# Kernel optimization log

Hardware: AMD Instinct MI355X
Metric: run time of the kernel (lower is better)

The kernel has to match this reference:

```python
import jax, jax.numpy as jnp
import numpy as np

B, D, H, K = 32768, 784, 500, 50


def setup_inputs() -> dict:
    key = jax.random.key(0)
    ks = jax.random.split(key, 12)
    s = 0.02  # weight init scale
    return {
        "x": jax.random.uniform(ks[0], (B, D), dtype=jnp.float32),
        "u": jax.random.uniform(ks[1], (B, K), dtype=jnp.float32),
        "enc_w1": jax.random.normal(ks[2], (D, H), dtype=jnp.float32) * s,
        "enc_b1": jnp.zeros((H,), jnp.float32),
        "w_alpha": jax.random.normal(ks[3], (H, K), dtype=jnp.float32) * s,
        "b_alpha": jnp.zeros((K,), jnp.float32),
        "w_beta": jax.random.normal(ks[4], (H, K), dtype=jnp.float32) * s,
        "b_beta": jnp.zeros((K,), jnp.float32),
        "dec_w1": jax.random.normal(ks[5], (K, H), dtype=jnp.float32) * s,
        "dec_b1": jnp.zeros((H,), jnp.float32),
        "dec_w2": jax.random.normal(ks[6], (H, D), dtype=jnp.float32) * s,
        "dec_b2": jnp.zeros((D,), jnp.float32),
    }


def reference(x, u, enc_w1, enc_b1, w_alpha, b_alpha, w_beta, b_beta,
              dec_w1, dec_b1, dec_w2, dec_b2):
    # encode
    h = jax.nn.relu(x @ enc_w1 + enc_b1)                       # [B,H]
    alpha = jax.nn.softplus(h @ w_alpha + b_alpha)             # [B,K] > 0
    beta = jax.nn.softplus(h @ w_beta + b_beta)                # [B,K] > 0
    # Kumaraswamy inverse-CDF sample: v = (1 - u^(1/beta))^(1/alpha)
    v = (1.0 - u ** (1.0 / beta)) ** (1.0 / alpha)             # [B,K]
    # stick-breaking: pi[k] = v[k] * prod_{j<k}(1 - v[j])  (exclusive cumprod)
    cp = jnp.cumprod(1.0 - v, axis=-1)                         # [B,K]
    pi = v * jnp.concatenate([jnp.ones_like(v[:, :1]), cp[:, :-1]], axis=-1)
    # decode
    hd = jax.nn.relu(pi @ dec_w1 + dec_b1)                     # [B,H]
    recon_x = jax.nn.sigmoid(hd @ dec_w2 + dec_b2)             # [B,D]
    return recon_x, alpha, beta
```

## Files before the change

kernel.cpp:

```cpp
#include <hip/hip_runtime.h>
#include <math.h>


typedef __bf16 bf16x8 __attribute__((ext_vector_type(8)));
typedef float f32x4 __attribute__((ext_vector_type(4)));

#define BATCH 32768
#define BM 128
#define BN 128
#define BK 64
#define NTHR 512

__device__ __forceinline__ unsigned short bf16_bits(float f) {
    __bf16 b = (__bf16)f;
    return __builtin_bit_cast(unsigned short, b);
}

__device__ __forceinline__ void gll16(const void* src, void* ldsdst) {
    __builtin_amdgcn_global_load_lds(
        (const __attribute__((address_space(1))) unsigned int*)src,
        (__attribute__((address_space(3))) unsigned int*)ldsdst,
        16, 0, 0);
}

template<int MODE>
__global__ __launch_bounds__(NTHR, 4) void mfma_gemm(
    const unsigned short* __restrict__ A,
    const unsigned short* __restrict__ Bt,
    const float* __restrict__ bias,
    void* __restrict__ Cv,
    int Kpad, int lda, int ldc, int Nreal, int nbx)
{
    __shared__ unsigned short As[BM * BK];
    __shared__ unsigned short Bs[BN * BK];

    const int nwg = gridDim.x;
    const int orig = blockIdx.x;
    const int q = nwg >> 3, r8 = nwg & 7;
    const int xcd = orig & 7;
    const int chunkbase = (xcd < r8) ? xcd * (q + 1) : r8 * (q + 1) + (xcd - r8) * q;
    const int wgid = chunkbase + (orig >> 3);
    const int bn = wgid % nbx;
    const size_t block_m = (size_t)(wgid / nbx) * BM;
    const int block_n = bn * BN;

    const int tid = threadIdx.x;
    const int l = tid & 63;
    const int wid = tid >> 6;
    const int wr = wid >> 2, wc = wid & 3;

    const int lr = l & 15;
    const int kh = l >> 4;

    f32x4 acc[4][2] = {};

    for (int k0 = 0; k0 < Kpad; k0 += BK) {
        #pragma unroll
        for (int i = 0; i < 2; ++i) {
            int chunk = wid * 2 + i;
            int gid = chunk * 64 + l;
            int r = gid >> 3;
            int kgs = (gid & 7) ^ (r & 7);
            gll16(Bt + (size_t)(block_n + r) * Kpad + k0 + kgs * 8, Bs + chunk * 512);
        }
        #pragma unroll
        for (int i = 0; i < 2; ++i) {
            int chunk = wid * 2 + i;
            int gid = chunk * 64 + l;
            int r = gid >> 3;
            int kgs = (gid & 7) ^ (r & 7);
            gll16(A + (block_m + r) * (size_t)lda + k0 + kgs * 8, As + chunk * 512);
        }
        __syncthreads();

        #pragma unroll
        for (int s = 0; s < 2; ++s) {
            bf16x8 af[4], bf[2];
            #pragma unroll
            for (int mi = 0; mi < 4; ++mi) {
                int row = wr * 64 + mi * 16 + lr;
                int g = (s * 4 + kh) ^ (row & 7);
                af[mi] = *(const bf16x8*)(As + row * 64 + g * 8);
            }
            #pragma unroll
            for (int ni = 0; ni < 2; ++ni) {
                int row = wc * 32 + ni * 16 + lr;
                int g = (s * 4 + kh) ^ (row & 7);
                bf[ni] = *(const bf16x8*)(Bs + row * 64 + g * 8);
            }
            #pragma unroll
            for (int mi = 0; mi < 4; ++mi)
                #pragma unroll
                for (int ni = 0; ni < 2; ++ni)
                    acc[mi][ni] = __builtin_amdgcn_mfma_f32_16x16x32_bf16(
                        af[mi], bf[ni], acc[mi][ni], 0, 0, 0);
        }
        __syncthreads();
    }

    const int rg = (l >> 4) * 4;
    #pragma unroll
    for (int mi = 0; mi < 4; ++mi) {
        #pragma unroll
        for (int ni = 0; ni < 2; ++ni) {
            int gn = block_n + wc * 32 + ni * 16 + lr;
            float bs = bias[gn];
            #pragma unroll
            for (int j = 0; j < 4; ++j) {
                long gm = block_m + wr * 64 + mi * 16 + rg + j;
                float z = acc[mi][ni][j] + bs;
                if (MODE == 0) {
                    z = fmaxf(z, 0.f);
                    ((unsigned short*)Cv)[gm * ldc + gn] = bf16_bits(z);
                } else if (MODE == 1) {
                    z = (z > 0.f) ? z + __logf(1.f + __expf(-z))
                                  : __logf(1.f + __expf(z));
                    float* out = (float*)Cv;
                    if (gn < 50)       out[gm * 50 + gn] = z;
                    else if (gn < 100) out[(size_t)BATCH * 50 + gm * 50 + (gn - 50)] = z;
                } else {
                    if (gn < Nreal) {
                        z = __fdividef(1.f, 1.f + __expf(-z));
                        ((float*)Cv)[gm * Nreal + gn] = z;
                    }
                }
            }
        }
    }
}

__global__ __launch_bounds__(NTHR, 4) void sample_gemm4(
    const float* __restrict__ u, const float* __restrict__ alpha,
    const float* __restrict__ beta,
    const unsigned short* __restrict__ dw1b,
    const float* __restrict__ biasd1,
    unsigned short* __restrict__ hdb)
{
    __shared__ unsigned short Pi[128 * 64];
    __shared__ unsigned short Wd[2][128 * 64];

    const int tid = threadIdx.x;
    const int l = tid & 63;
    const int wid = tid >> 6;

    const int nwg = gridDim.x;
    const int orig = blockIdx.x;
    const int q = nwg >> 3, r8 = nwg & 7;
    const int xcd = orig & 7;
    const int chunkbase = (xcd < r8) ? xcd * (q + 1) : r8 * (q + 1) + (xcd - r8) * q;
    const int wgid = chunkbase + (orig >> 3);
    const size_t block_m = (size_t)wgid * 128;

    auto stageW = [&](int j, int buf) {
        #pragma unroll
        for (int i = 0; i < 2; ++i) {
            int chunk = wid * 2 + i;
            int gid = chunk * 64 + l;
            int r = gid >> 3;
            int kgs = (gid & 7) ^ (r & 7);
            gll16(dw1b + (size_t)(j * 128 + r) * 64 + kgs * 8,
                  &Wd[buf][chunk * 512]);
        }
    };

    stageW(0, 0);

    for (int rr = 0; rr < 16; ++rr) {
        int row = wid * 16 + rr;
        size_t grow = block_m + row;
        float v = 0.f, w = 1.f;
        if (l < 50) {
            float a = alpha[grow * 50 + l];
            float b = beta[grow * 50 + l];
            float uu = u[grow * 50 + l];
            float t = exp2f(__fdividef(log2f(uu), b));
            v = exp2f(__fdividef(log2f(1.f - t), a));
            w = 1.f - v;
        }
        float p = w;
        #pragma unroll
        for (int off = 1; off < 64; off <<= 1) {
            float t2 = __shfl_up(p, off, 64);
            if (l >= off) p *= t2;
        }
        float ex = __shfl_up(p, 1, 64);
        if (l == 0) ex = 1.f;
        float pi = (l < 50) ? v * ex : 0.f;
        Pi[row * 64 + (((l >> 3) ^ (row & 7)) << 3) + (l & 7)] = bf16_bits(pi);
    }
    __syncthreads();

    const int lr = l & 15, kh = l >> 4;
    const int wr = wid >> 2, wc = wid & 3;
    const int rg = (l >> 4) * 4;

    for (int j = 0; j < 4; ++j) {
        if (j < 3) stageW(j + 1, (j + 1) & 1);
        f32x4 acc[4][2] = {};
        const unsigned short* W = Wd[j & 1];
        #pragma unroll
        for (int s = 0; s < 2; ++s) {
            bf16x8 af[4], bf[2];
            #pragma unroll
            for (int mi = 0; mi < 4; ++mi) {
                int row = wr * 64 + mi * 16 + lr;
                int g = (s * 4 + kh) ^ (row & 7);
                af[mi] = *(const bf16x8*)(Pi + row * 64 + g * 8);
            }
            #pragma unroll
            for (int ni = 0; ni < 2; ++ni) {
                int row = wc * 32 + ni * 16 + lr;
                int g = (s * 4 + kh) ^ (row & 7);
                bf[ni] = *(const bf16x8*)(W + row * 64 + g * 8);
            }
            #pragma unroll
            for (int mi = 0; mi < 4; ++mi)
                #pragma unroll
                for (int ni = 0; ni < 2; ++ni)
                    acc[mi][ni] = __builtin_amdgcn_mfma_f32_16x16x32_bf16(
                        af[mi], bf[ni], acc[mi][ni], 0, 0, 0);
        }
        #pragma unroll
        for (int mi = 0; mi < 4; ++mi) {
            #pragma unroll
            for (int ni = 0; ni < 2; ++ni) {
                int gn = j * 128 + wc * 32 + ni * 16 + lr;
                float bs = biasd1[gn];
                #pragma unroll
                for (int jj = 0; jj < 4; ++jj) {
                    long gm = block_m + wr * 64 + mi * 16 + rg + jj;
                    float z = fmaxf(acc[mi][ni][jj] + bs, 0.f);
                    hdb[gm * 512 + gn] = bf16_bits(z);
                }
            }
        }
        __syncthreads();
    }
}

__global__ __launch_bounds__(256) void cast_x(
    const float* __restrict__ x, unsigned short* __restrict__ xb)
{
    int gid = blockIdx.x * 256 + threadIdx.x;
    int r = gid / 104;
    int c = gid - r * 104;
    union { __bf16 b[8]; uint4 u; } pk;
    if (c < 98) {
        const float4* p = (const float4*)(x + (size_t)r * 784 + c * 8);
        float4 f0 = p[0], f1 = p[1];
        pk.b[0] = (__bf16)f0.x; pk.b[1] = (__bf16)f0.y;
        pk.b[2] = (__bf16)f0.z; pk.b[3] = (__bf16)f0.w;
        pk.b[4] = (__bf16)f1.x; pk.b[5] = (__bf16)f1.y;
        pk.b[6] = (__bf16)f1.z; pk.b[7] = (__bf16)f1.w;
    } else {
        pk.u = make_uint4(0, 0, 0, 0);
    }
    *(uint4*)(xb + (size_t)r * 832 + c * 8) = pk.u;
}

__global__ __launch_bounds__(256) void prep_all(
    const float* __restrict__ enc_w1, const float* __restrict__ enc_b1,
    const float* __restrict__ Wa, const float* __restrict__ ba,
    const float* __restrict__ Wb, const float* __restrict__ bb,
    const float* __restrict__ dec_w1, const float* __restrict__ dec_b1,
    const float* __restrict__ dec_w2, const float* __restrict__ dec_b2,
    unsigned short* __restrict__ w1b, float* __restrict__ bias1,
    unsigned short* __restrict__ wab, float* __restrict__ biasab,
    unsigned short* __restrict__ dw1b, float* __restrict__ biasd1,
    unsigned short* __restrict__ dw2b, float* __restrict__ biasd2)
{
    int bid = blockIdx.x;
    int t = threadIdx.x;
    if (bid < 1664) {
        int idx = bid * 256 + t;
        int n = idx / 832, k = idx - n * 832;
        float v = (n < 500 && k < 784) ? enc_w1[(size_t)k * 500 + n] : 0.f;
        w1b[idx] = bf16_bits(v);
        if (k == 0) bias1[n] = (n < 500) ? enc_b1[n] : 0.f;
    } else if (bid < 1920) {
        int idx = (bid - 1664) * 256 + t;
        int n = idx >> 9, k = idx & 511;
        float v = 0.f;
        if (k < 500) {
            if (n < 50)       v = Wa[(size_t)k * 50 + n];
            else if (n < 100) v = Wb[(size_t)k * 50 + (n - 50)];
        }
        wab[idx] = bf16_bits(v);
        if (k == 0) biasab[n] = (n < 50) ? ba[n] : ((n < 100) ? bb[n - 50] : 0.f);
    } else if (bid < 2048) {
        int idx = (bid - 1920) * 256 + t;
        int n = idx >> 6, k = idx & 63;
        float v = (n < 500 && k < 50) ? dec_w1[(size_t)k * 500 + n] : 0.f;
        dw1b[idx] = bf16_bits(v);
        if (k == 0) biasd1[n] = (n < 500) ? dec_b1[n] : 0.f;
    } else {
        int idx = (bid - 2048) * 256 + t;
        int n = idx >> 9, k = idx & 511;
        float v = (n < 784 && k < 500) ? dec_w2[(size_t)k * 784 + n] : 0.f;
        dw2b[idx] = bf16_bits(v);
        if (k == 0) biasd2[n] = (n < 784) ? dec_b2[n] : 0.f;
    }
}

extern "C" void kernel_launch(void* const* d_in, const int* in_sizes, int n_in,
                              void* d_out, int out_size, void* d_ws, size_t ws_size,
                              hipStream_t stream) {
    const float* x       = (const float*)d_in[0];
    const float* u       = (const float*)d_in[1];
    const float* enc_w1  = (const float*)d_in[2];
    const float* enc_b1  = (const float*)d_in[3];
    const float* w_alpha = (const float*)d_in[4];
    const float* b_alpha = (const float*)d_in[5];
    const float* w_beta  = (const float*)d_in[6];
    const float* b_beta  = (const float*)d_in[7];
    const float* dec_w1  = (const float*)d_in[8];
    const float* dec_b1  = (const float*)d_in[9];
    const float* dec_w2  = (const float*)d_in[10];
    const float* dec_b2  = (const float*)d_in[11];

    const int D = 784;

    float* out   = (float*)d_out;
    float* recon = out;
    float* alpha = out + (size_t)BATCH * D;

    unsigned short* xb = (unsigned short*)d_out;

    char* ws = (char*)d_ws;
    unsigned short* w1b  = (unsigned short*)(ws);
    unsigned short* wab  = (unsigned short*)(ws + 851968);
    unsigned short* dw1b = (unsigned short*)(ws + 983040);
    unsigned short* dw2b = (unsigned short*)(ws + 1048576);
    float* bias1  = (float*)(ws + 1966080);
    float* biasab = (float*)(ws + 1968128);
    float* biasd1 = (float*)(ws + 1970688);
    float* biasd2 = (float*)(ws + 1972736);
    unsigned short* h    = (unsigned short*)(ws + 2097152);
    unsigned short* hdb  = h;

    cast_x<<<dim3(BATCH * 104 / 256), 256, 0, stream>>>(x, xb);
    prep_all<<<dim3(3840), 256, 0, stream>>>(
        enc_w1, enc_b1, w_alpha, b_alpha, w_beta, b_beta,
        dec_w1, dec_b1, dec_w2, dec_b2,
        w1b, bias1, wab, biasab, dw1b, biasd1, dw2b, biasd2);

    mfma_gemm<0><<<dim3((512 / BN) * (BATCH / BM)), NTHR, 0, stream>>>(
        xb, w1b, bias1, h, 832, 832, 512, 500, 512 / BN);

    mfma_gemm<1><<<dim3(BATCH / BM), NTHR, 0, stream>>>(
        h, wab, biasab, alpha, 512, 512, 0, 100, 1);

    sample_gemm4<<<dim3(BATCH / 128), NTHR, 0, stream>>>(
        u, alpha, alpha + (size_t)BATCH * 50, dw1b, biasd1, hdb);

    mfma_gemm<2><<<dim3((896 / BN) * (BATCH / BM)), NTHR, 0, stream>>>(
        hdb, dw2b, biasd2, recon, 512, 512, 784, 784, 896 / BN);
}
```

Baseline: 150.8 us.

## Fuse alpha/beta GEMM with sampling and decoder GEMM; merge cast into prep

The softplus alpha/beta GEMM, the Kumaraswamy sampling with stick-breaking, and the first decoder GEMM now run in one kernel. Alpha and beta stay in LDS for the sampling step instead of being read back from global memory, though they are still written out as results. The x-cast kernel is folded into the weight-prep launch as extra blocks, so two kernel launches disappear in total. The fused kernel needs about 112KB of LDS, which reduces how many workgroups fit on each CU. The GEMM phase is also serialized with the sampling phase inside each block.

```diff
diff --git a/kernel.cpp b/kernel.cpp
--- a/kernel.cpp
+++ b/kernel.cpp
@@ -21,6 +21,13 @@
         (const __attribute__((address_space(1))) unsigned int*)src,
         (__attribute__((address_space(3))) unsigned int*)ldsdst,
         16, 0, 0);
+}
+
+__device__ __forceinline__ int xcd_swz(int orig, int nwg) {
+    int q = nwg >> 3, r8 = nwg & 7;
+    int xcd = orig & 7;
+    int chunkbase = (xcd < r8) ? xcd * (q + 1) : r8 * (q + 1) + (xcd - r8) * q;
+    return chunkbase + (orig >> 3);
 }
 
 template<int MODE>
@@ -34,12 +41,7 @@
     __shared__ unsigned short As[BM * BK];
     __shared__ unsigned short Bs[BN * BK];
 
-    const int nwg = gridDim.x;
-    const int orig = blockIdx.x;
-    const int q = nwg >> 3, r8 = nwg & 7;
-    const int xcd = orig & 7;
-    const int chunkbase = (xcd < r8) ? xcd * (q + 1) : r8 * (q + 1) + (xcd - r8) * q;
-    const int wgid = chunkbase + (orig >> 3);
+    const int wgid = xcd_swz(blockIdx.x, gridDim.x);
     const int bn = wgid % nbx;
     const size_t block_m = (size_t)(wgid / nbx) * BM;
     const int block_n = bn * BN;
@@ -48,7 +50,6 @@
     const int l = tid & 63;
     const int wid = tid >> 6;
     const int wr = wid >> 2, wc = wid & 3;
-
     const int lr = l & 15;
     const int kh = l >> 4;
 
@@ -72,7 +73,6 @@
             gll16(A + (block_m + r) * (size_t)lda + k0 + kgs * 8, As + chunk * 512);
         }
         __syncthreads();
-
         #pragma unroll
         for (int s = 0; s < 2; ++s) {
             bf16x8 af[4], bf[2];
@@ -112,12 +112,6 @@
                 if (MODE == 0) {
                     z = fmaxf(z, 0.f);
                     ((unsigned short*)Cv)[gm * ldc + gn] = bf16_bits(z);
-                } else if (MODE == 1) {
-                    z = (z > 0.f) ? z + __logf(1.f + __expf(-z))
-                                  : __logf(1.f + __expf(z));
-                    float* out = (float*)Cv;
-                    if (gn < 50)       out[gm * 50 + gn] = z;
-                    else if (gn < 100) out[(size_t)BATCH * 50 + gm * 50 + (gn - 50)] = z;
                 } else {
                     if (gn < Nreal) {
                         z = __fdividef(1.f, 1.f + __expf(-z));
@@ -129,51 +123,129 @@
     }
 }
 
-__global__ __launch_bounds__(NTHR, 4) void sample_gemm4(
-    const float* __restrict__ u, const float* __restrict__ alpha,
-    const float* __restrict__ beta,
+__global__ __launch_bounds__(NTHR, 2) void mid_fused(
+    const unsigned short* __restrict__ h,
+    const unsigned short* __restrict__ wab,
+    const float* __restrict__ biasab,
+    const float* __restrict__ u,
     const unsigned short* __restrict__ dw1b,
     const float* __restrict__ biasd1,
+    float* __restrict__ outAB,
     unsigned short* __restrict__ hdb)
 {
-    __shared__ unsigned short Pi[128 * 64];
-    __shared__ unsigned short Wd[2][128 * 64];
+    __shared__ __align__(16) unsigned char smem[114688];
+    float* ab = (float*)smem;
+    unsigned short* Pi = (unsigned short*)(smem + 65536);
+    unsigned short* Wd = (unsigned short*)(smem + 81920);
+    unsigned short* As = (unsigned short*)(smem + 81920);
+    unsigned short* Bs = (unsigned short*)(smem + 81920 + 16384);
 
     const int tid = threadIdx.x;
     const int l = tid & 63;
     const int wid = tid >> 6;
-
-    const int nwg = gridDim.x;
-    const int orig = blockIdx.x;
-    const int q = nwg >> 3, r8 = nwg & 7;
-    const int xcd = orig & 7;
-    const int chunkbase = (xcd < r8) ? xcd * (q + 1) : r8 * (q + 1) + (xcd - r8) * q;
-    const int wgid = chunkbase + (orig >> 3);
+    const int wr = wid >> 2, wc = wid & 3;
+    const int lr = l & 15;
+    const int kh = l >> 4;
+    const int rg = (l >> 4) * 4;
+
+    const int wgid = xcd_swz(blockIdx.x, gridDim.x);
     const size_t block_m = (size_t)wgid * 128;
 
-    auto stageW = [&](int j, int buf) {
+    {
+        f32x4 acc[4][2] = {};
+        for (int k0 = 0; k0 < 512; k0 += BK) {
+            #pragma unroll
+            for (int i = 0; i < 2; ++i) {
+                int chunk = wid * 2 + i;
+                int gid = chunk * 64 + l;
+                int r = gid >> 3;
+                int kgs = (gid & 7) ^ (r & 7);
+                gll16(wab + (size_t)r * 512 + k0 + kgs * 8, Bs + chunk * 512);
+            }
+            #pragma unroll
+            for (int i = 0; i < 2; ++i) {
+                int chunk = wid * 2 + i;
+                int gid = chunk * 64 + l;
+                int r = gid >> 3;
+                int kgs = (gid & 7) ^ (r & 7);
+                gll16(h + (block_m + r) * 512 + k0 + kgs * 8, As + chunk * 512);
+            }
+            __syncthreads();
+            #pragma unroll
+            for (int s = 0; s < 2; ++s) {
+                bf16x8 af[4], bf[2];
+                #pragma unroll
+                for (int mi = 0; mi < 4; ++mi) {
+                    int row = wr * 64 + mi * 16 + lr;
+                    int g = (s * 4 + kh) ^ (row & 7);
+                    af[mi] = *(const bf16x8*)(As + row * 64 + g * 8);
+                }
+                #pragma unroll
+                for (int ni = 0; ni < 2; ++ni) {
+                    int row = wc * 32 + ni * 16 + lr;
+                    int g = (s * 4 + kh) ^ (row & 7);
+                    bf[ni] = *(const bf16x8*)(Bs + row * 64 + g * 8);
+                }
+                #pragma unroll
+                for (int mi = 0; mi < 4; ++mi)
+                    #pragma unroll
+                    for (int ni = 0; ni < 2; ++ni)
+                        acc[mi][ni] = __builtin_amdgcn_mfma_f32_16x16x32_bf16(
+                            af[mi], bf[ni], acc[mi][ni], 0, 0, 0);
+            }
+            __syncthreads();
+        }
+
         #pragma unroll
         for (int i = 0; i < 2; ++i) {
             int chunk = wid * 2 + i;
             int gid = chunk * 64 + l;
             int r = gid >> 3;
             int kgs = (gid & 7) ^ (r & 7);
-            gll16(dw1b + (size_t)(j * 128 + r) * 64 + kgs * 8,
-                  &Wd[buf][chunk * 512]);
-        }
-    };
-
-    stageW(0, 0);
-
+            gll16(dw1b + (size_t)r * 64 + kgs * 8, Wd + chunk * 512);
+        }
+
+        #pragma unroll
+        for (int mi = 0; mi < 4; ++mi) {
+            #pragma unroll
+            for (int ni = 0; ni < 2; ++ni) {
+                int gn = wc * 32 + ni * 16 + lr;
+                float bs = biasab[gn];
+                #pragma unroll
+                for (int j = 0; j < 4; ++j) {
+                    int lm = wr * 64 + mi * 16 + rg + j;
+                    long gm = block_m + lm;
+                    float z = acc[mi][ni][j] + bs;
+                    z = (z > 0.f) ? z + __logf(1.f + __expf(-z))
+                                  : __logf(1.f + __expf(z));
+                    if (gn < 50) {
+                        outAB[gm * 50 + gn] = z;
+                        ab[lm * 64 + gn] = z;
+                    } else if (gn < 100) {
+                        outAB[(size_t)BATCH * 50 + gm * 50 + (gn - 50)] = z;
+                        ab[128 * 64 + lm * 64 + (gn - 50)] = z;
+                    }
+                }
+            }
+        }
+    }
+
+    float ur[16];
+    #pragma unroll
+    for (int rr = 0; rr < 16; ++rr) {
+        size_t grow = block_m + wid * 16 + rr;
+        ur[rr] = (l < 50) ? u[grow * 50 + l] : 0.5f;
+    }
+    __syncthreads();
+
+    #pragma unroll
     for (int rr = 0; rr < 16; ++rr) {
         int row = wid * 16 + rr;
-        size_t grow = block_m + row;
         float v = 0.f, w = 1.f;
         if (l < 50) {
-            float a = alpha[grow * 50 + l];
-            float b = beta[grow * 50 + l];
-            float uu = u[grow * 50 + l];
-            float t = exp2f(__fdividef(log2f(uu), b));
+            float a = ab[row * 64 + l];
+            float b = ab[128 * 64 + row * 64 + l];
+            float t = exp2f(__fdividef(log2f(ur[rr]), b));
             v = exp2f(__fdividef(log2f(1.f - t), a));
             w = 1.f - v;
         }
@@ -190,14 +262,21 @@
     }
     __syncthreads();
 
-    const int lr = l & 15, kh = l >> 4;
-    const int wr = wid >> 2, wc = wid & 3;
-    const int rg = (l >> 4) * 4;
-
     for (int j = 0; j < 4; ++j) {
-        if (j < 3) stageW(j + 1, (j + 1) & 1);
+        if (j < 3) {
+            int buf = (j + 1) & 1;
+            #pragma unroll
+            for (int i = 0; i < 2; ++i) {
+                int chunk = wid * 2 + i;
+                int gid = chunk * 64 + l;
+                int r = gid >> 3;
+                int kgs = (gid & 7) ^ (r & 7);
+                gll16(dw1b + (size_t)((j + 1) * 128 + r) * 64 + kgs * 8,
+                      Wd + buf * 8192 + chunk * 512);
+            }
+        }
         f32x4 acc[4][2] = {};
-        const unsigned short* W = Wd[j & 1];
+        const unsigned short* W = Wd + (j & 1) * 8192;
         #pragma unroll
         for (int s = 0; s < 2; ++s) {
             bf16x8 af[4], bf[2];
@@ -238,27 +317,8 @@
     }
 }
 
-__global__ __launch_bounds__(256) void cast_x(
-    const float* __restrict__ x, unsigned short* __restrict__ xb)
-{
-    int gid = blockIdx.x * 256 + threadIdx.x;
-    int r = gid / 104;
-    int c = gid - r * 104;
-    union { __bf16 b[8]; uint4 u; } pk;
-    if (c < 98) {
-        const float4* p = (const float4*)(x + (size_t)r * 784 + c * 8);
-        float4 f0 = p[0], f1 = p[1];
-        pk.b[0] = (__bf16)f0.x; pk.b[1] = (__bf16)f0.y;
-        pk.b[2] = (__bf16)f0.z; pk.b[3] = (__bf16)f0.w;
-        pk.b[4] = (__bf16)f1.x; pk.b[5] = (__bf16)f1.y;
-        pk.b[6] = (__bf16)f1.z; pk.b[7] = (__bf16)f1.w;
-    } else {
-        pk.u = make_uint4(0, 0, 0, 0);
-    }
-    *(uint4*)(xb + (size_t)r * 832 + c * 8) = pk.u;
-}
-
-__global__ __launch_bounds__(256) void prep_all(
+__global__ __launch_bounds__(256) void prep_cast(
+    const float* __restrict__ x, unsigned short* __restrict__ xb,
     const float* __restrict__ enc_w1, const float* __restrict__ enc_b1,
     const float* __restrict__ Wa, const float* __restrict__ ba,
     const float* __restrict__ Wb, const float* __restrict__ bb,
@@ -271,7 +331,23 @@
 {
     int bid = blockIdx.x;
     int t = threadIdx.x;
-    if (bid < 1664) {
+    if (bid >= 3840) {
+        int gid = (bid - 3840) * 256 + t;
+        int r = gid / 104;
+        int c = gid - r * 104;
+        union { __bf16 b[8]; uint4 u4; } pk;
+        if (c < 98) {
+            const float4* p = (const float4*)(x + (size_t)r * 784 + c * 8);
+            float4 f0 = p[0], f1 = p[1];
+            pk.b[0] = (__bf16)f0.x; pk.b[1] = (__bf16)f0.y;
+            pk.b[2] = (__bf16)f0.z; pk.b[3] = (__bf16)f0.w;
+            pk.b[4] = (__bf16)f1.x; pk.b[5] = (__bf16)f1.y;
+            pk.b[6] = (__bf16)f1.z; pk.b[7] = (__bf16)f1.w;
+        } else {
+            pk.u4 = make_uint4(0, 0, 0, 0);
+        }
+        *(uint4*)(xb + (size_t)r * 832 + c * 8) = pk.u4;
+    } else if (bid < 1664) {
         int idx = bid * 256 + t;
         int n = idx / 832, k = idx - n * 832;
         float v = (n < 500 && k < 784) ? enc_w1[(size_t)k * 500 + n] : 0.f;
@@ -338,20 +414,16 @@
     unsigned short* h    = (unsigned short*)(ws + 2097152);
     unsigned short* hdb  = h;
 
-    cast_x<<<dim3(BATCH * 104 / 256), 256, 0, stream>>>(x, xb);
-    prep_all<<<dim3(3840), 256, 0, stream>>>(
-        enc_w1, enc_b1, w_alpha, b_alpha, w_beta, b_beta,
+    prep_cast<<<dim3(3840 + BATCH * 104 / 256), 256, 0, stream>>>(
+        x, xb, enc_w1, enc_b1, w_alpha, b_alpha, w_beta, b_beta,
         dec_w1, dec_b1, dec_w2, dec_b2,
         w1b, bias1, wab, biasab, dw1b, biasd1, dw2b, biasd2);
 
     mfma_gemm<0><<<dim3((512 / BN) * (BATCH / BM)), NTHR, 0, stream>>>(
         xb, w1b, bias1, h, 832, 832, 512, 500, 512 / BN);
 
-    mfma_gemm<1><<<dim3(BATCH / BM), NTHR, 0, stream>>>(
-        h, wab, biasab, alpha, 512, 512, 0, 100, 1);
-
-    sample_gemm4<<<dim3(BATCH / 128), NTHR, 0, stream>>>(
-        u, alpha, alpha + (size_t)BATCH * 50, dw1b, biasd1, hdb);
+    mid_fused<<<dim3(BATCH / 128), NTHR, 0, stream>>>(
+        h, wab, biasab, u, dw1b, biasd1, alpha, hdb);
 
     mfma_gemm<2><<<dim3((896 / BN) * (BATCH / BM)), NTHR, 0, stream>>>(
         hdb, dw2b, biasd2, recon, 512, 512, 784, 784, 896 / BN);
```

Result: faster. 145.1 us (-3.8%).
